# Kernel optimization log

Hardware: AMD Instinct MI355X
Metric: run time of the kernel (lower is better)

The kernel has to match this reference:

```python
import jax, jax.numpy as jnp
import numpy as np


def setup_inputs() -> dict:
    key = jax.random.key(0)
    B, S, H, D = 2, 2048, 16, 64
    qkv = jax.random.normal(key, (B, S, 3, H, D), dtype=jnp.float32)
    return {"qkv_BxSx3xHxD": qkv}


def reference(qkv_BxSx3xHxD):
    # Two-step TTT with linear inner loop (eval mode: dropout_p = 0).
    q = qkv_BxSx3xHxD[:, :, 0]  # [B,S,H,D]
    k = qkv_BxSx3xHxD[:, :, 1]
    v = qkv_BxSx3xHxD[:, :, 2]
    # First causal linear-attention score matrix.
    a1 = jnp.tril(jnp.einsum('bthd,bshd->bhts', q, k))      # [B,H,S,S]
    # Intermediate output against K.
    o2 = jnp.einsum('bhts,bshd->bhtd', a1, k)                # [B,H,S,D]
    # Second causal score matrix from o2 vs K.
    a2 = jnp.tril(jnp.einsum('bhtd,bshd->bhts', o2, k))      # [B,H,S,S]
    a = 2.0 * a1 - a2                                        # fused correction
    return jnp.einsum('bhts,bshd->bthd', a, v)               # [B,S,H,D]
```

## Files before the change

kernel.cpp:

```cpp
#include <hip/hip_runtime.h>
#include <hip/hip_bf16.h>


typedef __bf16 bf16x8 __attribute__((ext_vector_type(8)));
typedef __bf16 bf16x2 __attribute__((ext_vector_type(2)));
typedef float  f32x4  __attribute__((ext_vector_type(4)));

#define MFMA16(a, b, c) __builtin_amdgcn_mfma_f32_16x16x32_bf16((a), (b), (c), 0, 0, 0)

static constexpr int S  = 2048;
static constexpr int H  = 16;
static constexpr int D  = 64;
static constexpr int RS = 3 * H * D;
static constexpr int BN = 64;
static constexpr int LR = 72;

__global__ __launch_bounds__(256, 2)
void ttt_kernel(const float* __restrict__ qkv, float* __restrict__ out)
{
    __shared__ __bf16 ldsS[128 * LR];
    __shared__ __bf16 ldsK[BN * LR];
    __shared__ __bf16 ldsW[D  * LR];

    const int tid  = threadIdx.x;
    const int wv   = tid >> 6;
    const int lane = tid & 63;
    const int q    = lane >> 4;
    const int l16  = lane & 15;

    const int i  = (int)blockIdx.x;
    const int p  = (i >> 3) & 15;
    const int bh = (i & 7) + 8 * (i >> 7);
    const int b  = bh >> 4;
    const int h  = bh & 15;
    const int tA = 64 * p;
    const int tB = 64 * (31 - p);
    const int nA = p + 1;
    const int nB = 32 - p;

    const float* baseQ = qkv + (size_t)b * S * RS + h * D;
    const float* baseK = baseQ + H * D;
    const float* baseV = baseQ + 2 * H * D;

    const int r2  = (tid >> 3) * 2;
    const int cb  = (tid & 7) * 8;
    const int cbK = cb ^ (((r2 >> 3) & 1) << 5);

    {
        const int r   = tid >> 1;
        const int gr  = (r < 64) ? (tA + r) : (tB + r - 64);
        const int cbq = (tid & 1) * 32;
        const float* pq = baseQ + (size_t)gr * RS + cbq;
        __bf16* dst = ldsS + r * LR + cbq;
#pragma unroll
        for (int u = 0; u < 4; ++u) {
            f32x4 f0 = *(const f32x4*)(pq + u * 8);
            f32x4 f1 = *(const f32x4*)(pq + u * 8 + 4);
            bf16x8 w;
#pragma unroll
            for (int j = 0; j < 4; ++j) { w[j] = (__bf16)f0[j]; w[4 + j] = (__bf16)f1[j]; }
            *(bf16x8*)(dst + u * 8) = w;
        }
    }

    f32x4 pk[4], pv[4];
    auto loadT = [&](f32x4* dst, const float* base, int s0) {
        const float* pg = base + (size_t)(s0 + r2) * RS + cb;
        dst[0] = *(const f32x4*)(pg);
        dst[1] = *(const f32x4*)(pg + 4);
        dst[2] = *(const f32x4*)(pg + RS);
        dst[3] = *(const f32x4*)(pg + RS + 4);
    };
    loadT(pk, baseK, 0);

    __syncthreads();

    bf16x8 Xf[2][2];
    const int rowA = wv * 16;
    const int rowB = 64 + wv * 16;
#pragma unroll
    for (int kt = 0; kt < 2; ++kt) {
        Xf[0][kt] = *(bf16x8*)(ldsS + (rowA + l16) * LR + kt * 32 + q * 8);
        Xf[1][kt] = *(bf16x8*)(ldsS + (rowB + l16) * LR + kt * 32 + q * 8);
    }
    __bf16* sA = ldsS + rowA * LR;
    __bf16* sB = ldsS + rowB * LR;

    const int rp   = (l16 >> 2) * 8 + (l16 & 3);
    const int kcol = (q * 8) | (((l16 >> 2) & 1) << 5);

    const f32x4 zero4 = {0.f, 0.f, 0.f, 0.f};
    f32x4 Y[2][4];
#pragma unroll
    for (int st = 0; st < 2; ++st)
#pragma unroll
        for (int nd = 0; nd < 4; ++nd) Y[st][nd] = zero4;

    const int tgA = tA + wv * 16 + l16;
    const int tgB = tB + wv * 16 + l16;

    for (int pass = 0; pass < 2; ++pass) {
        for (int sb = 0; sb < nB; ++sb) {
            const bool actA = (sb < nA);
            __syncthreads();
            {
                bf16x8 w0, w1;
#pragma unroll
                for (int j = 0; j < 4; ++j) {
                    w0[j] = (__bf16)pk[0][j]; w0[4 + j] = (__bf16)pk[1][j];
                    w1[j] = (__bf16)pk[2][j]; w1[4 + j] = (__bf16)pk[3][j];
                }
                *(bf16x8*)(ldsK + r2 * LR + cbK)       = w0;
                *(bf16x8*)(ldsK + (r2 + 1) * LR + cbK) = w1;
                f32x4* src = (pass == 0) ? pk : pv;
#pragma unroll
                for (int j = 0; j < 8; ++j) {
                    const int d = cb + j;
                    bf16x2 w;
                    w[0] = (__bf16)((j < 4) ? src[0][j & 3] : src[1][j & 3]);
                    w[1] = (__bf16)((j < 4) ? src[2][j & 3] : src[3][j & 3]);
                    *(bf16x2*)(ldsW + d * LR + (r2 ^ (d & 56))) = w;
                }
            }
            __syncthreads();

            if (sb + 1 < nB) {
                loadT(pk, baseK, (sb + 1) * BN);
                if (pass == 1) loadT(pv, baseV, (sb + 1) * BN);
            } else if (pass == 0) {
                loadT(pk, baseK, 0);
                loadT(pv, baseV, 0);
            }

            f32x4 PtA[4], PtB[4];
#pragma unroll
            for (int mi = 0; mi < 4; ++mi) { PtA[mi] = zero4; PtB[mi] = zero4; }
#pragma unroll
            for (int kt = 0; kt < 2; ++kt) {
#pragma unroll
                for (int mi = 0; mi < 4; ++mi) {
                    bf16x8 kf = *(bf16x8*)(ldsK
                        + ((mi >> 1) * 32 + (mi & 1) * 4 + rp) * LR
                        + ((kt * 32) ^ kcol));
                    PtB[mi] = MFMA16(kf, Xf[1][kt], PtB[mi]);
                    if (actA) PtA[mi] = MFMA16(kf, Xf[0][kt], PtA[mi]);
                }
            }

            bf16x8 afA[2], afB[2];
            {
                const bool diagB = (sb == nB - 1);
#pragma unroll
                for (int kt = 0; kt < 2; ++kt) {
                    bf16x8 a;
                    if (diagB) {
#pragma unroll
                        for (int b2 = 0; b2 < 2; ++b2)
#pragma unroll
                            for (int r = 0; r < 4; ++r) {
                                const int sg = sb * BN + kt * 32 + q * 8 + b2 * 4 + r;
                                a[b2 * 4 + r] = (sg <= tgB) ? (__bf16)PtB[2 * kt + b2][r]
                                                            : (__bf16)0.0f;
                            }
                    } else {
#pragma unroll
                        for (int b2 = 0; b2 < 2; ++b2)
#pragma unroll
                            for (int r = 0; r < 4; ++r)
                                a[b2 * 4 + r] = (__bf16)PtB[2 * kt + b2][r];
                    }
                    afB[kt] = a;
                }
                if (actA) {
                    const bool diagA = (sb == nA - 1);
#pragma unroll
                    for (int kt = 0; kt < 2; ++kt) {
                        bf16x8 a;
                        if (diagA) {
#pragma unroll
                            for (int b2 = 0; b2 < 2; ++b2)
#pragma unroll
                                for (int r = 0; r < 4; ++r) {
                                    const int sg = sb * BN + kt * 32 + q * 8 + b2 * 4 + r;
                                    a[b2 * 4 + r] = (sg <= tgA) ? (__bf16)PtA[2 * kt + b2][r]
                                                                : (__bf16)0.0f;
                                }
                        } else {
#pragma unroll
                            for (int b2 = 0; b2 < 2; ++b2)
#pragma unroll
                                for (int r = 0; r < 4; ++r)
                                    a[b2 * 4 + r] = (__bf16)PtA[2 * kt + b2][r];
                        }
                        afA[kt] = a;
                    }
                }
            }

#pragma unroll
            for (int kt = 0; kt < 2; ++kt) {
#pragma unroll
                for (int nd = 0; nd < 4; ++nd) {
                    const int d = l16 + nd * 16;
                    bf16x8 wf = *(bf16x8*)(ldsW + d * LR + ((kt * 32 + q * 8) ^ (d & 56)));
                    Y[1][nd] = MFMA16(afB[kt], wf, Y[1][nd]);
                    if (actA) Y[0][nd] = MFMA16(afA[kt], wf, Y[0][nd]);
                }
            }
        }

        if (pass == 0) {
#pragma unroll
            for (int st = 0; st < 2; ++st) {
                __bf16* sc = (st == 0) ? sA : sB;
#pragma unroll
                for (int nd = 0; nd < 4; ++nd)
#pragma unroll
                    for (int r = 0; r < 4; ++r)
                        sc[(q * 4 + r) * LR + l16 + nd * 16] = (__bf16)Y[st][nd][r];
#pragma unroll
                for (int kt = 0; kt < 2; ++kt) {
                    bf16x8 of = *(bf16x8*)(sc + l16 * LR + kt * 32 + q * 8);
#pragma unroll
                    for (int j = 0; j < 8; ++j)
                        Xf[st][kt][j] = (__bf16)(2.0f * (float)Xf[st][kt][j] - (float)of[j]);
                }
#pragma unroll
                for (int nd = 0; nd < 4; ++nd) Y[st][nd] = zero4;
            }
        } else {
#pragma unroll
            for (int st = 0; st < 2; ++st) {
                const int tb = (st == 0) ? tA : tB;
#pragma unroll
                for (int nd = 0; nd < 4; ++nd)
#pragma unroll
                    for (int r = 0; r < 4; ++r) {
                        const int t = tb + wv * 16 + q * 4 + r;
                        const int d = l16 + nd * 16;
                        out[(((size_t)b * S + t) * H + h) * D + d] = Y[st][nd][r];
                    }
            }
        }
    }
}

extern "C" void kernel_launch(void* const* d_in, const int* in_sizes, int n_in,
                              void* d_out, int out_size, void* d_ws, size_t ws_size,
                              hipStream_t stream)
{
    const float* qkv = (const float*)d_in[0];
    float* out = (float*)d_out;
    ttt_kernel<<<dim3(512), 256, 0, stream>>>(qkv, out);
}
```

Before: 161.5 us.

## Double-buffer K/W LDS tiles and flatten both passes into one loop

Splits the K and W shared-memory tiles into two buffers and merges the two passes into a single loop over 2*nB steps. Each step computes from the current buffer while the next tile's converted data is written into the other buffer. This leaves one barrier per step instead of two, which is meant to cut synchronisation stalls between the LDS commit and the MFMA work. The cost is extra LDS per block, and the flattened loop adds some control logic for pass transitions.

```diff
diff --git a/kernel.cpp b/kernel.cpp
--- a/kernel.cpp
+++ b/kernel.cpp
@@ -19,8 +19,8 @@
 void ttt_kernel(const float* __restrict__ qkv, float* __restrict__ out)
 {
     __shared__ __bf16 ldsS[128 * LR];
-    __shared__ __bf16 ldsK[BN * LR];
-    __shared__ __bf16 ldsW[D  * LR];
+    __shared__ __bf16 ldsK[2][BN * LR];
+    __shared__ __bf16 ldsW[2][D  * LR];
 
     const int tid  = threadIdx.x;
     const int wv   = tid >> 6;
@@ -71,6 +71,26 @@
         dst[2] = *(const f32x4*)(pg + RS);
         dst[3] = *(const f32x4*)(pg + RS + 4);
     };
+
+    auto commit = [&](__bf16* K_, __bf16* W_, const f32x4* src) {
+        bf16x8 w0, w1;
+#pragma unroll
+        for (int j = 0; j < 4; ++j) {
+            w0[j] = (__bf16)pk[0][j]; w0[4 + j] = (__bf16)pk[1][j];
+            w1[j] = (__bf16)pk[2][j]; w1[4 + j] = (__bf16)pk[3][j];
+        }
+        *(bf16x8*)(K_ + r2 * LR + cbK)       = w0;
+        *(bf16x8*)(K_ + (r2 + 1) * LR + cbK) = w1;
+#pragma unroll
+        for (int j = 0; j < 8; ++j) {
+            const int d = cb + j;
+            bf16x2 w;
+            w[0] = (__bf16)((j < 4) ? src[0][j & 3] : src[1][j & 3]);
+            w[1] = (__bf16)((j < 4) ? src[2][j & 3] : src[3][j & 3]);
+            *(bf16x2*)(W_ + d * LR + (r2 ^ (d & 56))) = w;
+        }
+    };
+
     loadT(pk, baseK, 0);
 
     __syncthreads();
@@ -99,67 +119,78 @@
     const int tgA = tA + wv * 16 + l16;
     const int tgB = tB + wv * 16 + l16;
 
-    for (int pass = 0; pass < 2; ++pass) {
-        for (int sb = 0; sb < nB; ++sb) {
-            const bool actA = (sb < nA);
-            __syncthreads();
-            {
-                bf16x8 w0, w1;
-#pragma unroll
-                for (int j = 0; j < 4; ++j) {
-                    w0[j] = (__bf16)pk[0][j]; w0[4 + j] = (__bf16)pk[1][j];
-                    w1[j] = (__bf16)pk[2][j]; w1[4 + j] = (__bf16)pk[3][j];
+    commit(ldsK[0], ldsW[0], pk);
+    __syncthreads();
+
+    const int NT = 2 * nB;
+
+    for (int u = 0; u < NT; ++u) {
+        const int c    = u & 1;
+        const int pass = (u >= nB) ? 1 : 0;
+        const int sb   = u - (pass ? nB : 0);
+        const bool actA = (sb < nA);
+
+        if (u + 1 < NT) {
+            const int np  = (u + 1 >= nB) ? 1 : 0;
+            const int nsb = (u + 1) - (np ? nB : 0);
+            loadT(pk, baseK, nsb * BN);
+            if (np) loadT(pv, baseV, nsb * BN);
+        }
+
+        __bf16* K_ = ldsK[c];
+        __bf16* W_ = ldsW[c];
+
+        f32x4 PtA[4], PtB[4];
+#pragma unroll
+        for (int mi = 0; mi < 4; ++mi) { PtA[mi] = zero4; PtB[mi] = zero4; }
+#pragma unroll
+        for (int kt = 0; kt < 2; ++kt) {
+#pragma unroll
+            for (int mi = 0; mi < 4; ++mi) {
+                bf16x8 kf = *(bf16x8*)(K_
+                    + ((mi >> 1) * 32 + (mi & 1) * 4 + rp) * LR
+                    + ((kt * 32) ^ kcol));
+                PtB[mi] = MFMA16(kf, Xf[1][kt], PtB[mi]);
+                if (actA) PtA[mi] = MFMA16(kf, Xf[0][kt], PtA[mi]);
+            }
+        }
+
+        bf16x8 afA[2], afB[2];
+        {
+            const bool diagB = (sb == nB - 1);
+#pragma unroll
+            for (int kt = 0; kt < 2; ++kt) {
+                bf16x8 a;
+                if (diagB) {
+#pragma unroll
+                    for (int b2 = 0; b2 < 2; ++b2)
+#pragma unroll
+                        for (int r = 0; r < 4; ++r) {
+                            const int sg = sb * BN + kt * 32 + q * 8 + b2 * 4 + r;
+                            a[b2 * 4 + r] = (sg <= tgB) ? (__bf16)PtB[2 * kt + b2][r]
+                                                        : (__bf16)0.0f;
+                        }
+                } else {
+#pragma unroll
+                    for (int b2 = 0; b2 < 2; ++b2)
+#pragma unroll
+                        for (int r = 0; r < 4; ++r)
+                            a[b2 * 4 + r] = (__bf16)PtB[2 * kt + b2][r];
                 }
-                *(bf16x8*)(ldsK + r2 * LR + cbK)       = w0;
-                *(bf16x8*)(ldsK + (r2 + 1) * LR + cbK) = w1;
-                f32x4* src = (pass == 0) ? pk : pv;
-#pragma unroll
-                for (int j = 0; j < 8; ++j) {
-                    const int d = cb + j;
-                    bf16x2 w;
-                    w[0] = (__bf16)((j < 4) ? src[0][j & 3] : src[1][j & 3]);
-                    w[1] = (__bf16)((j < 4) ? src[2][j & 3] : src[3][j & 3]);
-                    *(bf16x2*)(ldsW + d * LR + (r2 ^ (d & 56))) = w;
-                }
-            }
-            __syncthreads();
-
-            if (sb + 1 < nB) {
-                loadT(pk, baseK, (sb + 1) * BN);
-                if (pass == 1) loadT(pv, baseV, (sb + 1) * BN);
-            } else if (pass == 0) {
-                loadT(pk, baseK, 0);
-                loadT(pv, baseV, 0);
-            }
-
-            f32x4 PtA[4], PtB[4];
-#pragma unroll
-            for (int mi = 0; mi < 4; ++mi) { PtA[mi] = zero4; PtB[mi] = zero4; }
-#pragma unroll
-            for (int kt = 0; kt < 2; ++kt) {
-#pragma unroll
-                for (int mi = 0; mi < 4; ++mi) {
-                    bf16x8 kf = *(bf16x8*)(ldsK
-                        + ((mi >> 1) * 32 + (mi & 1) * 4 + rp) * LR
-                        + ((kt * 32) ^ kcol));
-                    PtB[mi] = MFMA16(kf, Xf[1][kt], PtB[mi]);
-                    if (actA) PtA[mi] = MFMA16(kf, Xf[0][kt], PtA[mi]);
-                }
-            }
-
-            bf16x8 afA[2], afB[2];
-            {
-                const bool diagB = (sb == nB - 1);
+                afB[kt] = a;
+            }
+            if (actA) {
+                const bool diagA = (sb == nA - 1);
 #pragma unroll
                 for (int kt = 0; kt < 2; ++kt) {
                     bf16x8 a;
-                    if (diagB) {
+                    if (diagA) {
 #pragma unroll
                         for (int b2 = 0; b2 < 2; ++b2)
 #pragma unroll
                             for (int r = 0; r < 4; ++r) {
                                 const int sg = sb * BN + kt * 32 + q * 8 + b2 * 4 + r;
-                                a[b2 * 4 + r] = (sg <= tgB) ? (__bf16)PtB[2 * kt + b2][r]
+                                a[b2 * 4 + r] = (sg <= tgA) ? (__bf16)PtA[2 * kt + b2][r]
                                                             : (__bf16)0.0f;
                             }
                     } else {
@@ -167,49 +198,25 @@
                         for (int b2 = 0; b2 < 2; ++b2)
 #pragma unroll
                             for (int r = 0; r < 4; ++r)
-                                a[b2 * 4 + r] = (__bf16)PtB[2 * kt + b2][r];
+                                a[b2 * 4 + r] = (__bf16)PtA[2 * kt + b2][r];
                     }
-                    afB[kt] = a;
+                    afA[kt] = a;
                 }
-                if (actA) {
-                    const bool diagA = (sb == nA - 1);
-#pragma unroll
-                    for (int kt = 0; kt < 2; ++kt) {
-                        bf16x8 a;
-                        if (diagA) {
-#pragma unroll
-                            for (int b2 = 0; b2 < 2; ++b2)
-#pragma unroll
-                                for (int r = 0; r < 4; ++r) {
-                                    const int sg = sb * BN + kt * 32 + q * 8 + b2 * 4 + r;
-                                    a[b2 * 4 + r] = (sg <= tgA) ? (__bf16)PtA[2 * kt + b2][r]
-                                                                : (__bf16)0.0f;
-                                }
-                        } else {
-#pragma unroll
-                            for (int b2 = 0; b2 < 2; ++b2)
-#pragma unroll
-                                for (int r = 0; r < 4; ++r)
-                                    a[b2 * 4 + r] = (__bf16)PtA[2 * kt + b2][r];
-                        }
-                        afA[kt] = a;
-                    }
-                }
-            }
-
-#pragma unroll
-            for (int kt = 0; kt < 2; ++kt) {
-#pragma unroll
-                for (int nd = 0; nd < 4; ++nd) {
-                    const int d = l16 + nd * 16;
-                    bf16x8 wf = *(bf16x8*)(ldsW + d * LR + ((kt * 32 + q * 8) ^ (d & 56)));
-                    Y[1][nd] = MFMA16(afB[kt], wf, Y[1][nd]);
-                    if (actA) Y[0][nd] = MFMA16(afA[kt], wf, Y[0][nd]);
-                }
-            }
-        }
-
-        if (pass == 0) {
+            }
+        }
+
+#pragma unroll
+        for (int kt = 0; kt < 2; ++kt) {
+#pragma unroll
+            for (int nd = 0; nd < 4; ++nd) {
+                const int d = l16 + nd * 16;
+                bf16x8 wf = *(bf16x8*)(W_ + d * LR + ((kt * 32 + q * 8) ^ (d & 56)));
+                Y[1][nd] = MFMA16(afB[kt], wf, Y[1][nd]);
+                if (actA) Y[0][nd] = MFMA16(afA[kt], wf, Y[0][nd]);
+            }
+        }
+
+        if (u == nB - 1) {
 #pragma unroll
             for (int st = 0; st < 2; ++st) {
                 __bf16* sc = (st == 0) ? sA : sB;
@@ -228,7 +235,7 @@
 #pragma unroll
                 for (int nd = 0; nd < 4; ++nd) Y[st][nd] = zero4;
             }
-        } else {
+        } else if (u == NT - 1) {
 #pragma unroll
             for (int st = 0; st < 2; ++st) {
                 const int tb = (st == 0) ? tA : tB;
@@ -241,6 +248,11 @@
                         out[(((size_t)b * S + t) * H + h) * D + d] = Y[st][nd][r];
                     }
             }
+        }
+
+        if (u + 1 < NT) {
+            commit(ldsK[1 - c], ldsW[1 - c], (u + 1 >= nB) ? pv : pk);
+            __syncthreads();
         }
     }
 }
```

New measurement: 158.3 us. 2.0% less time.
